# Kernel optimization log

Measured on AMD Instinct MI355X. Metric: run time of the kernel, lower is better.

The kernel has to match this reference:

```python
import jax, jax.numpy as jnp
import numpy as np

N_GENE, N_DRUG = 20000, 3000
D_GENE, D_DRUG = 1024, 512
H = [256, 128]
E_GG, E_DD, E_DT = 600000, 120000, 150000
P_DROP = 0.2


def _dropout(x, key):
    # F.dropout(p=0.2, training=True) with a fixed key for determinism
    keep = jax.random.bernoulli(key, 1.0 - P_DROP, x.shape)
    return jnp.where(keep, x / (1.0 - P_DROP), 0.0).astype(x.dtype)


def _gcn_norm(x, W, b, edge_index, n):
    src, dst = edge_index[0], edge_index[1]
    loops = jnp.arange(n, dtype=src.dtype)
    src = jnp.concatenate([src, loops])
    dst = jnp.concatenate([dst, loops])
    deg = jax.ops.segment_sum(jnp.ones(src.shape, x.dtype), dst, num_segments=n)
    dinv = jax.lax.rsqrt(deg)  # deg >= 1 thanks to self loops
    xw = x @ W  # [n_src, out]
    msg = xw[src] * (dinv[src] * dinv[dst])[:, None]  # [E+n, out]
    return jax.ops.segment_sum(msg, dst, num_segments=n) + b


def _gcn_plain(x, W, b, edge_index, n_dst):
    # PyG GCNConv(add_self_loops=False, normalize=False): A X W + b (bipartite scatter)
    xw = x @ W
    return jax.ops.segment_sum(xw[edge_index[0]], edge_index[1], num_segments=n_dst) + b


def _l2norm(x):
    # F.normalize(dim=1, p=2), eps=1e-12
    n = jnp.linalg.norm(x, axis=1, keepdims=True)
    return x / jnp.maximum(n, 1e-12)


def setup_inputs() -> dict:
    key = jax.random.key(0)
    ks = jax.random.split(key, 32)
    inp = {}
    inp["gene_feat"] = jax.random.normal(ks[0], (N_GENE, D_GENE), jnp.float32)
    inp["drug_feat"] = jax.random.normal(ks[1], (N_DRUG, D_DRUG), jnp.float32)
    inp["ei_gg"] = jax.random.randint(ks[2], (2, E_GG), 0, N_GENE)
    inp["ei_dd"] = jax.random.randint(ks[3], (2, E_DD), 0, N_DRUG)
    # drug_target: messages from drug (src row) to gene (dst row)
    inp["ei_dt"] = jnp.stack([jax.random.randint(ks[4], (E_DT,), 0, N_DRUG),
                               jax.random.randint(ks[5], (E_DT,), 0, N_GENE)])
    # target_drug: messages from gene (src row) to drug (dst row)
    inp["ei_td"] = jnp.stack([jax.random.randint(ks[6], (E_DT,), 0, N_GENE),
                               jax.random.randint(ks[7], (E_DT,), 0, N_DRUG)])
    dims_in = {"gg": D_GENE, "dd": D_DRUG, "dt": D_DRUG, "td": D_GENE}
    i = 8
    for l, h in enumerate(H):
        for et in ["gg", "dd", "dt", "td"]:
            din = dims_in[et] if l == 0 else H[l - 1]
            s = float(1.0 / np.sqrt(din))
            inp[f"W{l}_{et}"] = jax.random.uniform(ks[i], (din, h), jnp.float32, -s, s)
            i += 1
            inp[f"b{l}_{et}"] = jnp.zeros((h,), jnp.float32)
    return inp


def reference(gene_feat, drug_feat, ei_gg, ei_dd, ei_dt, ei_td,
              W0_gg, b0_gg, W0_dd, b0_dd, W0_dt, b0_dt, W0_td, b0_td,
              W1_gg, b1_gg, W1_dd, b1_dd, W1_dt, b1_dt, W1_td, b1_td):
    dk = jax.random.split(jax.random.key(42), 8)
    layers = [
        ((W0_gg, b0_gg), (W0_dd, b0_dd), (W0_dt, b0_dt), (W0_td, b0_td)),
        ((W1_gg, b1_gg), (W1_dd, b1_dd), (W1_dt, b1_dt), (W1_td, b1_td)),
    ]
    xg, xd = gene_feat, drug_feat
    k = 0
    for (Wgg, bgg), (Wdd, bdd), (Wdt, bdt), (Wtd, btd) in layers:
        gg = jax.nn.relu(_gcn_norm(_dropout(xg, dk[k + 0]), Wgg, bgg, ei_gg, N_GENE))
        dd = jax.nn.relu(_gcn_norm(_dropout(xd, dk[k + 1]), Wdd, bdd, ei_dd, N_DRUG))
        dt = jax.nn.relu(_gcn_plain(_dropout(xd, dk[k + 2]), Wdt, bdt, ei_dt, N_GENE))
        td = jax.nn.relu(_gcn_plain(_dropout(xg, dk[k + 3]), Wtd, btd, ei_td, N_DRUG))
        # per-edge-type L2 normalize, then sum contributions per node type
        xg = _l2norm(gg) + _l2norm(dt)
        xd = _l2norm(dd) + _l2norm(td)
        k += 4
    # concat node-type outputs: genes first, drugs second -> [N_GENE+N_DRUG, H[-1]]
    return jnp.concatenate([xg, xd], axis=0)
```

## Files before the change

kernel.cpp:

```cpp
#include <hip/hip_runtime.h>
#include <stdint.h>

#define N_GENE 20000
#define N_DRUG 3000
#define D_GENE 1024
#define D_DRUG 512
#define H0 256
#define H1 128
#define E_GG 600000
#define E_DD 120000
#define E_DT 150000

typedef __attribute__((ext_vector_type(8))) short bf16x8;
typedef __attribute__((ext_vector_type(4))) float f32x4;

__host__ __device__ inline uint32_t rotl32(uint32_t x, int d) {
#ifdef __HIP_DEVICE_COMPILE__
    return __builtin_amdgcn_alignbit(x, x, 32 - d);
#else
    return (x << d) | (x >> (32 - d));
#endif
}

__host__ __device__ inline void tf2x32(uint32_t k0, uint32_t k1, uint32_t x0, uint32_t x1,
                                       uint32_t& o0, uint32_t& o1) {
    uint32_t ks2 = k0 ^ k1 ^ 0x1BD11BDAu;
    x0 += k0; x1 += k1;
#define TFR(r) { x0 += x1; x1 = rotl32(x1, r); x1 ^= x0; }
    TFR(13) TFR(15) TFR(26) TFR(6)
    x0 += k1; x1 += ks2 + 1u;
    TFR(17) TFR(29) TFR(16) TFR(24)
    x0 += ks2; x1 += k0 + 2u;
    TFR(13) TFR(15) TFR(26) TFR(6)
    x0 += k0; x1 += k1 + 3u;
    TFR(17) TFR(29) TFR(16) TFR(24)
    x0 += k1; x1 += ks2 + 4u;
    TFR(13) TFR(15) TFR(26) TFR(6)
    x0 += ks2; x1 += k0 + 5u;
#undef TFR
    o0 = x0; o1 = x1;
}

__device__ inline float bf_lo(uint32_t u) { return __uint_as_float(u << 16); }
__device__ inline float bf_hi(uint32_t u) { return __uint_as_float(u & 0xFFFF0000u); }

__device__ inline bool tf_keep(unsigned idx, uint32_t k0, uint32_t k1) {
    uint32_t a, b;
    tf2x32(k0, k1, 0u, idx, a, b);
    return (((a ^ b) >> 9) < 6710887u);
}
__device__ inline uint32_t bfbits(float x) {
    uint32_t u = __float_as_uint(x);
    return ((u + 0x7FFFu + ((u >> 16) & 1u)) >> 16) & 0xFFFFu;
}

__device__ inline short f2bf(float f) {
    uint32_t u = __float_as_uint(f);
    uint32_t r = (u + 0x7FFFu + ((u >> 16) & 1u)) >> 16;
    return (short)r;
}

#define CUM_E0 600000u
#define CUM_E1 720000u
#define CUM_E2 870000u
#define CUM_E3 1020000u

struct CastT4P {
    unsigned c0, c1, c2, c3;
    int lgK0, lgK1, lgK2, lgK3;
    int N;
};
__device__ inline void castT_body(unsigned idx, const float* W0, const float* W1,
                                  const float* W2, const float* W3,
                                  short* __restrict__ Wt, const CastT4P& P) {
    if (idx >= P.c3) return;
    unsigned base; const float* W; int lgK;
    if (idx >= P.c2)      { base = P.c2; W = W3; lgK = P.lgK3; }
    else if (idx >= P.c1) { base = P.c1; W = W2; lgK = P.lgK2; }
    else if (idx >= P.c0) { base = P.c0; W = W1; lgK = P.lgK1; }
    else                  { base = 0u;   W = W0; lgK = P.lgK0; }
    unsigned local = idx - base;
    unsigned n = local >> lgK, k = local & ((1u << lgK) - 1u);
    Wt[idx] = f2bf(W[(size_t)k * P.N + n]);
}

__global__ __launch_bounds__(256) void count4x_kernel(
    const int* __restrict__ gg, const int* __restrict__ dd,
    const int* __restrict__ dt, const int* __restrict__ td, int* __restrict__ cnt,
    const float* __restrict__ W0, const float* __restrict__ W1,
    const float* __restrict__ W2, const float* __restrict__ W3,
    short* __restrict__ Wt, CastT4P P, int countBlocks) {
    int bx = blockIdx.x;
    if (bx >= countBlocks) {
        castT_body((unsigned)(bx - countBlocks) * 256u + threadIdx.x, W0, W1, W2, W3, Wt, P);
        return;
    }
    unsigned e = (unsigned)bx * 256u + threadIdx.x;
    if (e >= CUM_E3) return;
    const int* dsts; unsigned base, noff;
    if (e >= CUM_E2)      { dsts = td + E_DT; base = CUM_E2; noff = 43000; }
    else if (e >= CUM_E1) { dsts = dt + E_DT; base = CUM_E1; noff = 23000; }
    else if (e >= CUM_E0) { dsts = dd + E_DD; base = CUM_E0; noff = 20000; }
    else                  { dsts = gg + E_GG; base = 0;      noff = 0; }
    atomicAdd(&cnt[noff + dsts[e - base]], 1);
}

__global__ __launch_bounds__(1024) void scan_p1(const int* __restrict__ cnt,
                                                int* __restrict__ tmp, int* __restrict__ bsum) {
    __shared__ int buf[1024];
    int tid = threadIdx.x;
    int i = blockIdx.x * 1024 + tid;
    int v = (i < 46000) ? cnt[i] : 0;
    buf[tid] = v;
    __syncthreads();
    for (int off = 1; off < 1024; off <<= 1) {
        int t = (tid >= off) ? buf[tid - off] : 0;
        __syncthreads();
        buf[tid] += t;
        __syncthreads();
    }
    if (i < 46000) tmp[i] = buf[tid];
    if (tid == 1023) bsum[blockIdx.x] = buf[1023];
}

__global__ void scan_p2(int* __restrict__ bsum) {
    int lane = threadIdx.x;
    int v = (lane < 45) ? bsum[lane] : 0;
    int orig = v;
    for (int off = 1; off < 64; off <<= 1) {
        int t = __shfl_up(v, off, 64);
        if (lane >= off) v += t;
    }
    if (lane < 45) bsum[lane] = v - orig;
}

__global__ __launch_bounds__(1024) void scan_p3(const int* __restrict__ cnt,
                                                const int* __restrict__ tmp,
                                                const int* __restrict__ bsum,
                                                int* __restrict__ rpall, int* __restrict__ pos,
                                                float* __restrict__ dinv_g,
                                                float* __restrict__ dinv_d) {
    int i = blockIdx.x * 1024 + threadIdx.x;
    if (i < 46000) {
        int g = tmp[i] - cnt[i] + bsum[blockIdx.x];
        rpall[i] = g;
        pos[i] = g;
        if (i < 20000) dinv_g[i] = 1.0f / sqrtf((float)cnt[i] + 1.0f);
        else if (i < 23000) dinv_d[i - 20000] = 1.0f / sqrtf((float)cnt[i] + 1.0f);
    }
    if (i == 0) rpall[46000] = (int)CUM_E3;
}

__global__ __launch_bounds__(256) void fill_kernel(
    const int* __restrict__ gg, const int* __restrict__ dd,
    const int* __restrict__ dt, const int* __restrict__ td,
    int* __restrict__ pos, int* __restrict__ col) {
    unsigned e = blockIdx.x * 256u + threadIdx.x;
    if (e >= CUM_E3) return;
    const int* ei; unsigned base, noff; int E;
    if (e >= CUM_E2)      { ei = td; base = CUM_E2; noff = 43000; E = E_DT; }
    else if (e >= CUM_E1) { ei = dt; base = CUM_E1; noff = 23000; E = E_DT; }
    else if (e >= CUM_E0) { ei = dd; base = CUM_E0; noff = 20000; E = E_DD; }
    else                  { ei = gg; base = 0;      noff = 0;     E = E_GG; }
    unsigned local = e - base;
    int src = ei[local], dst = ei[E + local];
    int p = atomicAdd(&pos[noff + dst], 1);
    col[p] = src;
}

struct GDescF { const float* X; unsigned boff, coff; const float* rs; int M, K, mb0; uint32_t k0, k1; };
#define LDP 72
template <int BN>
__global__ __launch_bounds__(256, 2) void gemmf_kernel(
    const short* __restrict__ Wb, short* __restrict__ Cb,
    GDescF d0, GDescF d1, GDescF d2, GDescF d3) {
    constexpr int WN = BN / 4;
    constexpr int NF = WN / 16;
    __shared__ short As[32 * LDP];
    GDescF d;
    int bx = blockIdx.x;
    if (bx >= d3.mb0) d = d3;
    else if (bx >= d2.mb0) d = d2;
    else if (bx >= d1.mb0) d = d1;
    else d = d0;
    bx -= d.mb0;
    const int M = d.M, K = d.K;
    const short* Bt = Wb + d.boff;
    short* C = Cb + d.coff;
    const uint32_t k0 = d.k0, k1 = d.k1;

    int tid = threadIdx.x;
    int lane = tid & 63, w = tid >> 6;
    int m = lane & 15, kb = lane >> 4;
    int n0w = w * WN;
    int gm = bx * 32;

    int ar = tid >> 3, ac = (tid & 7) * 8;
    int agr = min(gm + ar, M - 1);
    const float* pax = d.X + (size_t)agr * K + ac;
    unsigned abase = (unsigned)agr * (unsigned)K + (unsigned)ac;
    int aslot = ar * LDP + ac;
    const short* pbf = Bt + (size_t)(n0w + m) * K + kb * 8;
    const size_t bfrag = (size_t)16 * K;

    f32x4 acc[2][NF];
#pragma unroll
    for (int i = 0; i < 2; i++)
#pragma unroll
        for (int j = 0; j < NF; j++) acc[i][j] = (f32x4){0.f, 0.f, 0.f, 0.f};

    int nt = K >> 6;
    for (int t = 0; t < nt; ++t) {
        int kt = t << 6;
        float4 xa = *(const float4*)(pax + kt);
        float4 xb = *(const float4*)(pax + kt + 4);
        unsigned li = abase + (unsigned)kt;
        bool e0 = tf_keep(li + 0u, k0, k1), e1 = tf_keep(li + 1u, k0, k1);
        bool e2 = tf_keep(li + 2u, k0, k1), e3 = tf_keep(li + 3u, k0, k1);
        bool e4 = tf_keep(li + 4u, k0, k1), e5 = tf_keep(li + 5u, k0, k1);
        bool e6 = tf_keep(li + 6u, k0, k1), e7 = tf_keep(li + 7u, k0, k1);
        uint32_t w0 = (e0 ? bfbits(xa.x) : 0u) | ((e1 ? bfbits(xa.y) : 0u) << 16);
        uint32_t w1 = (e2 ? bfbits(xa.z) : 0u) | ((e3 ? bfbits(xa.w) : 0u) << 16);
        uint32_t w2 = (e4 ? bfbits(xb.x) : 0u) | ((e5 ? bfbits(xb.y) : 0u) << 16);
        uint32_t w3 = (e6 ? bfbits(xb.z) : 0u) | ((e7 ? bfbits(xb.w) : 0u) << 16);
        __syncthreads();
        *(uint4*)&As[aslot] = make_uint4(w0, w1, w2, w3);
        __syncthreads();
#pragma unroll
        for (int ks = 0; ks < 2; ++ks) {
            bf16x8 a0 = *(const bf16x8*)&As[m * LDP + ks * 32 + kb * 8];
            bf16x8 a1 = *(const bf16x8*)&As[(16 + m) * LDP + ks * 32 + kb * 8];
#pragma unroll
            for (int nf = 0; nf < NF; nf++) {
                bf16x8 bf = *(const bf16x8*)(pbf + nf * bfrag + kt + ks * 32);
                acc[0][nf] = __builtin_amdgcn_mfma_f32_16x16x32_bf16(a0, bf, acc[0][nf], 0, 0, 0);
                acc[1][nf] = __builtin_amdgcn_mfma_f32_16x16x32_bf16(a1, bf, acc[1][nf], 0, 0, 0);
            }
        }
    }
#pragma unroll
    for (int mf = 0; mf < 2; ++mf)
#pragma unroll
        for (int j = 0; j < 4; ++j) {
            int r = gm + mf * 16 + kb * 4 + j;
            if (r < M) {
                float s = (d.rs ? d.rs[r] : 1.0f) * 1.25f;
#pragma unroll
                for (int nf = 0; nf < NF; ++nf)
                    C[(size_t)r * BN + n0w + nf * 16 + m] = f2bf(acc[mf][nf][j] * s);
            }
        }
}

struct AggP {
    const short* XWa; const int* rpa; const float* dinv; const float* ba;
    const short* XWb; const int* rpb; const float* bb;
    float* out; int n_dst;
};

template <int F>
__device__ inline void agg_body(const AggP& P, const int* __restrict__ col, int row, int lane) {
    const int h = 64 * F;
    int c0 = lane * F;
    float acc[F], va[F];

#pragma unroll
    for (int i = 0; i < F; i++) acc[i] = 0.f;
    {
        if constexpr (F == 4) {
            uint2 u = *(const uint2*)(P.XWa + (size_t)row * h + c0);
            acc[0] += bf_lo(u.x); acc[1] += bf_hi(u.x);
            acc[2] += bf_lo(u.y); acc[3] += bf_hi(u.y);
        } else {
            uint32_t u = *(const uint32_t*)(P.XWa + (size_t)row * h + c0);
            acc[0] += bf_lo(u); acc[1] += bf_hi(u);
        }
        int s0 = P.rpa[row], s1 = P.rpa[row + 1];
        int p = s0;
        for (; p + 8 <= s1; p += 8) {
            int c[8];
#pragma unroll
            for (int i = 0; i < 8; i++) c[i] = col[p + i];
            if constexpr (F == 4) {
                uint2 g[8];
#pragma unroll
                for (int i = 0; i < 8; i++) g[i] = *(const uint2*)(P.XWa + (size_t)c[i] * h + c0);
#pragma unroll
                for (int i = 0; i < 8; i++) {
                    acc[0] += bf_lo(g[i].x); acc[1] += bf_hi(g[i].x);
                    acc[2] += bf_lo(g[i].y); acc[3] += bf_hi(g[i].y);
                }
            } else {
                uint32_t g[8];
#pragma unroll
                for (int i = 0; i < 8; i++) g[i] = *(const uint32_t*)(P.XWa + (size_t)c[i] * h + c0);
#pragma unroll
                for (int i = 0; i < 8; i++) { acc[0] += bf_lo(g[i]); acc[1] += bf_hi(g[i]); }
            }
        }
        for (; p < s1; p++) {
            int s = col[p];
            if constexpr (F == 4) {
                uint2 u = *(const uint2*)(P.XWa + (size_t)s * h + c0);
                acc[0] += bf_lo(u.x); acc[1] += bf_hi(u.x);
                acc[2] += bf_lo(u.y); acc[3] += bf_hi(u.y);
            } else {
                uint32_t u = *(const uint32_t*)(P.XWa + (size_t)s * h + c0);
                acc[0] += bf_lo(u); acc[1] += bf_hi(u);
            }
        }
    }
    float mul = P.dinv[row];
    float ssa = 0.f;
#pragma unroll
    for (int i = 0; i < F; i++) {
        float v = fmaxf(acc[i] * mul + P.ba[c0 + i], 0.f);
        va[i] = v;
        ssa += v * v;
    }

#pragma unroll
    for (int i = 0; i < F; i++) acc[i] = 0.f;
    {
        int s0 = P.rpb[row], s1 = P.rpb[row + 1];
        int p = s0;
        for (; p + 8 <= s1; p += 8) {
            int c[8];
#pragma unroll
            for (int i = 0; i < 8; i++) c[i] = col[p + i];
            if constexpr (F == 4) {
                uint2 g[8];
#pragma unroll
                for (int i = 0; i < 8; i++) g[i] = *(const uint2*)(P.XWb + (size_t)c[i] * h + c0);
#pragma unroll
                for (int i = 0; i < 8; i++) {
                    acc[0] += bf_lo(g[i].x); acc[1] += bf_hi(g[i].x);
                    acc[2] += bf_lo(g[i].y); acc[3] += bf_hi(g[i].y);
                }
            } else {
                uint32_t g[8];
#pragma unroll
                for (int i = 0; i < 8; i++) g[i] = *(const uint32_t*)(P.XWb + (size_t)c[i] * h + c0);
#pragma unroll
                for (int i = 0; i < 8; i++) { acc[0] += bf_lo(g[i]); acc[1] += bf_hi(g[i]); }
            }
        }
        for (; p < s1; p++) {
            int s = col[p];
            if constexpr (F == 4) {
                uint2 u = *(const uint2*)(P.XWb + (size_t)s * h + c0);
                acc[0] += bf_lo(u.x); acc[1] += bf_hi(u.x);
                acc[2] += bf_lo(u.y); acc[3] += bf_hi(u.y);
            } else {
                uint32_t u = *(const uint32_t*)(P.XWb + (size_t)s * h + c0);
                acc[0] += bf_lo(u); acc[1] += bf_hi(u);
            }
        }
    }
    float ssb = 0.f;
#pragma unroll
    for (int i = 0; i < F; i++) {
        float v = fmaxf(acc[i] + P.bb[c0 + i], 0.f);
        acc[i] = v;
        ssb += v * v;
    }

#pragma unroll
    for (int off = 32; off >= 1; off >>= 1) {
        ssa += __shfl_xor(ssa, off, 64);
        ssb += __shfl_xor(ssb, off, 64);
    }
    float sa = 1.0f / fmaxf(sqrtf(ssa), 1e-12f);
    float sb = 1.0f / fmaxf(sqrtf(ssb), 1e-12f);
    float* orow = P.out + (size_t)row * h + c0;
    if constexpr (F == 4) {
        *(float4*)orow = make_float4(va[0] * sa + acc[0] * sb, va[1] * sa + acc[1] * sb,
                                     va[2] * sa + acc[2] * sb, va[3] * sa + acc[3] * sb);
    } else {
        *(float2*)orow = make_float2(va[0] * sa + acc[0] * sb, va[1] * sa + acc[1] * sb);
    }
}

template <int F, bool TAIL>
__global__ __launch_bounds__(256) void agg2x_kernel(
    AggP pg, AggP pd, const int* __restrict__ col, int geneBlocks, int aggBlocks,
    const float* W0, const float* W1, const float* W2, const float* W3,
    short* Wt, CastT4P tp) {
    int bx = blockIdx.x;
    if (TAIL && bx >= aggBlocks) {
        castT_body((unsigned)(bx - aggBlocks) * 256u + threadIdx.x, W0, W1, W2, W3, Wt, tp);
        return;
    }
    int lane = threadIdx.x & 63;
    if (bx < geneBlocks) {
        int row = bx * 4 + (threadIdx.x >> 6);
        if (row < pg.n_dst) agg_body<F>(pg, col, row, lane);
    } else {
        int row = (bx - geneBlocks) * 4 + (threadIdx.x >> 6);
        if (row < pd.n_dst) agg_body<F>(pd, col, row, lane);
    }
}

extern "C" void kernel_launch(void* const* d_in, const int* in_sizes, int n_in,
                              void* d_out, int out_size, void* d_ws, size_t ws_size,
                              hipStream_t stream) {
    const float* gene = (const float*)d_in[0];
    const float* drug = (const float*)d_in[1];
    const int* ei_gg = (const int*)d_in[2];
    const int* ei_dd = (const int*)d_in[3];
    const int* ei_dt = (const int*)d_in[4];
    const int* ei_td = (const int*)d_in[5];
    const float* W0gg = (const float*)d_in[6];  const float* b0gg = (const float*)d_in[7];
    const float* W0dd = (const float*)d_in[8];  const float* b0dd = (const float*)d_in[9];
    const float* W0dt = (const float*)d_in[10]; const float* b0dt = (const float*)d_in[11];
    const float* W0td = (const float*)d_in[12]; const float* b0td = (const float*)d_in[13];
    const float* W1gg = (const float*)d_in[14]; const float* b1gg = (const float*)d_in[15];
    const float* W1dd = (const float*)d_in[16]; const float* b1dd = (const float*)d_in[17];
    const float* W1dt = (const float*)d_in[18]; const float* b1dt = (const float*)d_in[19];
    const float* W1td = (const float*)d_in[20]; const float* b1td = (const float*)d_in[21];

    uint32_t dk[8][2];
    for (uint32_t i = 0; i < 8; i++) tf2x32(0u, 42u, 0u, i, dk[i][0], dk[i][1]);

    char* p = (char*)d_ws;
    auto take = [&](size_t bytes) -> void* {
        void* r = (void*)p;
        p += (bytes + 255) & ~(size_t)255;
        return r;
    };
    short* XW   = (short*)take(sizeof(short) * 11776000ULL);
    short* Wt0  = (short*)take(sizeof(short) * 786432ULL);
    short* Wt1  = (short*)take(sizeof(short) * 131072ULL);
    float* xg1  = (float*)take(sizeof(float) * (size_t)N_GENE * H0);
    float* xd1  = (float*)take(sizeof(float) * (size_t)N_DRUG * H0);
    float* dinv_g = (float*)take(sizeof(float) * N_GENE);
    float* dinv_d = (float*)take(sizeof(float) * N_DRUG);
    int* cnt   = (int*)take(4 * 46000);
    int* tmp   = (int*)take(4 * 46000);
    int* bsum  = (int*)take(4 * 64);
    int* pos   = (int*)take(4 * 46000);
    int* rpall = (int*)take(4 * 46001);
    int* col   = (int*)take(4 * 1020000);

    const int* rp_gg = rpall;
    const int* rp_dd = rpall + 20000;
    const int* rp_dt = rpall + 23000;
    const int* rp_td = rpall + 43000;

    hipMemsetAsync(cnt, 0, 4 * 46000, stream);
    CastT4P tp0 = {262144u, 524288u, 655360u, 786432u, 10, 10, 9, 9, H0};
    int countBlocks = (1020000 + 255) / 256;
    count4x_kernel<<<countBlocks + (786432 + 255) / 256, 256, 0, stream>>>(
        ei_gg, ei_dd, ei_dt, ei_td, cnt, W0gg, W0td, W0dd, W0dt, Wt0, tp0, countBlocks);
    scan_p1<<<45, 1024, 0, stream>>>(cnt, tmp, bsum);
    scan_p2<<<1, 64, 0, stream>>>(bsum);
    scan_p3<<<45, 1024, 0, stream>>>(cnt, tmp, bsum, rpall, pos, dinv_g, dinv_d);
    fill_kernel<<<(1020000 + 255) / 256, 256, 0, stream>>>(ei_gg, ei_dd, ei_dt, ei_td, pos, col);

    {
        GDescF g0 = {gene, 0u,      0u,        dinv_g,  N_GENE, 1024, 0,    dk[0][0], dk[0][1]};
        GDescF g1 = {gene, 262144u, 5120000u,  nullptr, N_GENE, 1024, 625,  dk[3][0], dk[3][1]};
        GDescF g2 = {drug, 524288u, 10240000u, dinv_d,  N_DRUG, 512,  1250, dk[1][0], dk[1][1]};
        GDescF g3 = {drug, 655360u, 11008000u, nullptr, N_DRUG, 512,  1344, dk[2][0], dk[2][1]};
        gemmf_kernel<256><<<1438, 256, 0, stream>>>(Wt0, XW, g0, g1, g2, g3);

        AggP pg = {XW, rp_gg, dinv_g, b0gg, XW + 11008000, rp_dt, b0dt, xg1, N_GENE};
        AggP pd = {XW + 10240000, rp_dd, dinv_d, b0dd, XW + 5120000, rp_td, b0td, xd1, N_DRUG};
        CastT4P tp1 = {32768u, 65536u, 98304u, 131072u, 8, 8, 8, 8, H1};
        int geneBlocks = (N_GENE + 3) / 4, aggBlocks = geneBlocks + (N_DRUG + 3) / 4;
        agg2x_kernel<4, true><<<aggBlocks + (131072 + 255) / 256, 256, 0, stream>>>(
            pg, pd, col, geneBlocks, aggBlocks, W1gg, W1td, W1dd, W1dt, Wt1, tp1);
    }

    {
        GDescF g0 = {xg1, 0u,     0u,        dinv_g,  N_GENE, 256, 0,    dk[4][0], dk[4][1]};
        GDescF g1 = {xg1, 32768u, 5120000u,  nullptr, N_GENE, 256, 625,  dk[7][0], dk[7][1]};
        GDescF g2 = {xd1, 65536u, 10240000u, dinv_d,  N_DRUG, 256, 1250, dk[5][0], dk[5][1]};
        GDescF g3 = {xd1, 98304u, 11008000u, nullptr, N_DRUG, 256, 1344, dk[6][0], dk[6][1]};
        gemmf_kernel<128><<<1438, 256, 0, stream>>>(Wt1, XW, g0, g1, g2, g3);

        float* og = (float*)d_out;
        float* od = og + (size_t)N_GENE * H1;
        AggP pg = {XW, rp_gg, dinv_g, b1gg, XW + 11008000, rp_dt, b1dt, og, N_GENE};
        AggP pd = {XW + 10240000, rp_dd, dinv_d, b1dd, XW + 5120000, rp_td, b1td, od, N_DRUG};
        CastT4P tpDummy = {0u, 0u, 0u, 0u, 0, 0, 0, 0, 0};
        int geneBlocks = (N_GENE + 3) / 4, aggBlocks = geneBlocks + (N_DRUG + 3) / 4;
        agg2x_kernel<2, false><<<aggBlocks, 256, 0, stream>>>(
            pg, pd, col, geneBlocks, aggBlocks,
            nullptr, nullptr, nullptr, nullptr, nullptr, tpDummy);
    }
}
```

Baseline: 420.4 us.

## Stage weight tiles in shared memory and shrink GEMM K-tile to 32

The fused dropout GEMM now loads the bf16 weight (B) tile cooperatively into LDS each iteration instead of having every wave read its B fragments straight from global memory. The K step drops from 64 to 32, which halves the A staging per thread and removes the padded LDS stride. The aim is to replace redundant, poorly coalesced global B reads with one coalesced load per tile. In exchange it doubles the number of loop iterations and barriers, and the unpadded 32-short row stride may cause LDS bank conflicts.

```diff
diff --git a/kernel.cpp b/kernel.cpp
--- a/kernel.cpp
+++ b/kernel.cpp
@@ -169,14 +169,15 @@
 }
 
 struct GDescF { const float* X; unsigned boff, coff; const float* rs; int M, K, mb0; uint32_t k0, k1; };
-#define LDP 72
 template <int BN>
 __global__ __launch_bounds__(256, 2) void gemmf_kernel(
     const short* __restrict__ Wb, short* __restrict__ Cb,
     GDescF d0, GDescF d1, GDescF d2, GDescF d3) {
     constexpr int WN = BN / 4;
     constexpr int NF = WN / 16;
-    __shared__ short As[32 * LDP];
+    constexpr int TPR = 256 / BN;
+    __shared__ short As[32 * 32];
+    __shared__ short Bs[BN * 32];
     GDescF d;
     int bx = blockIdx.x;
     if (bx >= d3.mb0) d = d3;
@@ -195,13 +196,15 @@
     int n0w = w * WN;
     int gm = bx * 32;
 
-    int ar = tid >> 3, ac = (tid & 7) * 8;
+    int ar = tid >> 3, ac = (tid & 7) * 4;
     int agr = min(gm + ar, M - 1);
     const float* pax = d.X + (size_t)agr * K + ac;
     unsigned abase = (unsigned)agr * (unsigned)K + (unsigned)ac;
-    int aslot = ar * LDP + ac;
-    const short* pbf = Bt + (size_t)(n0w + m) * K + kb * 8;
-    const size_t bfrag = (size_t)16 * K;
+    int awslot = ar * 32 + ac;
+    int brow = tid / TPR;
+    int bcol = (tid % TPR) * (32 / TPR);
+    const short* pb = Bt + (size_t)brow * K + bcol;
+    int bwslot = brow * 32 + bcol;
 
     f32x4 acc[2][NF];
 #pragma unroll
@@ -209,30 +212,41 @@
 #pragma unroll
         for (int j = 0; j < NF; j++) acc[i][j] = (f32x4){0.f, 0.f, 0.f, 0.f};
 
-    int nt = K >> 6;
+    int nt = K >> 5;
     for (int t = 0; t < nt; ++t) {
-        int kt = t << 6;
+        int kt = t << 5;
         float4 xa = *(const float4*)(pax + kt);
-        float4 xb = *(const float4*)(pax + kt + 4);
+        uint4 b0 = *(const uint4*)(pb + kt);
+        uint4 b1, b2, b3;
+        if constexpr (TPR == 1) {
+            b1 = *(const uint4*)(pb + kt + 8);
+            b2 = *(const uint4*)(pb + kt + 16);
+            b3 = *(const uint4*)(pb + kt + 24);
+        } else {
+            b1 = *(const uint4*)(pb + kt + 8);
+        }
         unsigned li = abase + (unsigned)kt;
         bool e0 = tf_keep(li + 0u, k0, k1), e1 = tf_keep(li + 1u, k0, k1);
         bool e2 = tf_keep(li + 2u, k0, k1), e3 = tf_keep(li + 3u, k0, k1);
-        bool e4 = tf_keep(li + 4u, k0, k1), e5 = tf_keep(li + 5u, k0, k1);
-        bool e6 = tf_keep(li + 6u, k0, k1), e7 = tf_keep(li + 7u, k0, k1);
         uint32_t w0 = (e0 ? bfbits(xa.x) : 0u) | ((e1 ? bfbits(xa.y) : 0u) << 16);
         uint32_t w1 = (e2 ? bfbits(xa.z) : 0u) | ((e3 ? bfbits(xa.w) : 0u) << 16);
-        uint32_t w2 = (e4 ? bfbits(xb.x) : 0u) | ((e5 ? bfbits(xb.y) : 0u) << 16);
-        uint32_t w3 = (e6 ? bfbits(xb.z) : 0u) | ((e7 ? bfbits(xb.w) : 0u) << 16);
         __syncthreads();
-        *(uint4*)&As[aslot] = make_uint4(w0, w1, w2, w3);
+        *(uint2*)&As[awslot] = make_uint2(w0, w1);
+        *(uint4*)&Bs[bwslot] = b0;
+        if constexpr (TPR == 1) {
+            *(uint4*)&Bs[bwslot + 8] = b1;
+            *(uint4*)&Bs[bwslot + 16] = b2;
+            *(uint4*)&Bs[bwslot + 24] = b3;
+        } else {
+            *(uint4*)&Bs[bwslot + 8] = b1;
+        }
         __syncthreads();
-#pragma unroll
-        for (int ks = 0; ks < 2; ++ks) {
-            bf16x8 a0 = *(const bf16x8*)&As[m * LDP + ks * 32 + kb * 8];
-            bf16x8 a1 = *(const bf16x8*)&As[(16 + m) * LDP + ks * 32 + kb * 8];
+        {
+            bf16x8 a0 = *(const bf16x8*)&As[m * 32 + kb * 8];
+            bf16x8 a1 = *(const bf16x8*)&As[(16 + m) * 32 + kb * 8];
 #pragma unroll
             for (int nf = 0; nf < NF; nf++) {
-                bf16x8 bf = *(const bf16x8*)(pbf + nf * bfrag + kt + ks * 32);
+                bf16x8 bf = *(const bf16x8*)&Bs[(n0w + nf * 16 + m) * 32 + kb * 8];
                 acc[0][nf] = __builtin_amdgcn_mfma_f32_16x16x32_bf16(a0, bf, acc[0][nf], 0, 0, 0);
                 acc[1][nf] = __builtin_amdgcn_mfma_f32_16x16x32_bf16(a1, bf, acc[1][nf], 0, 0, 0);
             }
```

After: 414.8 us. No clear change (-1.3%).
